# Performance work log

Hardware: AMD Instinct MI355X
Metric: run time of the kernel (lower is better)

The kernel has to match this reference:

```python
import jax, jax.numpy as jnp
import numpy as np

# LLRDenoiser config (init_kwargs): ndim=2, patch W=8, stride S=4, ths=0.1, rand_shift=False
P = 8      # patch size (isotropic)
STRIDE = 4 # patch stride
THS = 0.1  # soft-threshold on singular values
B, C, H, W = 2, 16, 512, 512  # batch, coefficient axis, spatial dims


def setup_inputs() -> dict:
    key = jax.random.key(0)
    x = jax.random.normal(key, (B, C, H, W), dtype=jnp.float32)
    return {"x": x}


def _patch_idx(n, p, s):
    # start indices for sliding windows, inclusive of last full window
    starts = jnp.arange(0, n - p + 1, s)
    return starts[:, None] + jnp.arange(p)[None, :]  # (n_patches, p)


def _llr_denoise(x):
    idx_h = _patch_idx(H, P, STRIDE)  # (nH, P)
    idx_w = _patch_idx(W, P, STRIDE)  # (nW, P)
    nH, nW = idx_h.shape[0], idx_w.shape[0]
    hi = idx_h[:, None, :, None]  # (nH, 1, P, 1)
    wi = idx_w[None, :, None, :]  # (1, nW, 1, P)

    # extract overlapping patches -> (B, C, nH, nW, P, P)
    patches = x[:, :, hi, wi]
    # Casorati matrices per patch: (B, nH*nW, C, P*P)
    mats = patches.transpose(0, 2, 3, 1, 4, 5).reshape(B, nH * nW, C, P * P)

    # batched thin SVD + soft-threshold of singular values
    u, s, vh = jnp.linalg.svd(mats, full_matrices=False)
    s_st = jnp.sign(s) * jnp.maximum(jnp.abs(s) - THS, 0.0)
    mats = (u * s_st[..., None, :]) @ vh

    # back to patch layout (B, C, nH, nW, P, P)
    patches = mats.reshape(B, nH, nW, C, P, P).transpose(0, 3, 1, 2, 4, 5)

    # overlap-add reconstruction, averaged by patch coverage count
    out = jnp.zeros_like(x).at[:, :, hi, wi].add(patches)
    cnt = jnp.zeros((H, W), x.dtype).at[hi[..., 0, :, :] if False else idx_h[:, None, :, None], idx_w[None, :, None, :]].add(1.0)
    return out / cnt


def reference(x):
    return _llr_denoise(x)
```

## Files before the change

kernel.cpp:

```cpp
#include <hip/hip_runtime.h>


#define NBATCH  2
#define NCH     16
#define HDIM    512
#define WDIM    512
#define NPH     127
#define NPW     127
#define NPATCH  (NBATCH * NPH * NPW)
#define NCELL   128
#define THS     0.1f
#define NSIT    8

typedef short bf16x8 __attribute__((ext_vector_type(8)));
typedef float f32x4  __attribute__((ext_vector_type(4)));

#define MFMA(a,b,c) __builtin_amdgcn_mfma_f32_16x16x32_bf16((a),(b),(c),0,0,0)

static __device__ inline short f2bf(float x) {
  return __builtin_bit_cast(short, (__bf16)x);
}
static __device__ inline float blo2f(unsigned int v) {
  return __builtin_bit_cast(float, v << 16);
}
static __device__ inline float bhi2f(unsigned int v) {
  return __builtin_bit_cast(float, v & 0xffff0000u);
}
static __device__ inline unsigned int pack2bf(float lo, float hi) {
  unsigned int a = (unsigned short)f2bf(lo);
  unsigned int b = (unsigned short)f2bf(hi);
  return (b << 16) | a;
}

static __device__ inline int xcd_swz(int b, int nwg) {
  const int q = nwg >> 3, r = nwg & 7;
  const int x = b & 7, lo = b >> 3;
  return (x < r ? x * (q + 1) : r * (q + 1) + (x - r) * q) + lo;
}

static __device__ inline bf16x8 fragc(f32x4 v) {
  bf16x8 r;
  r[0] = f2bf(v[0]); r[1] = f2bf(v[1]); r[2] = f2bf(v[2]); r[3] = f2bf(v[3]);
  r[4] = 0; r[5] = 0; r[6] = 0; r[7] = 0;
  return r;
}

#define ZS_NBLK ((NPATCH + 3) / 4)
__global__ __launch_bounds__(256) void llr_zs(const float* __restrict__ x,
                                              uint2* __restrict__ zs) {
  const int blk = xcd_swz(blockIdx.x, ZS_NBLK);
  const int pid = blk * 4 + (threadIdx.x >> 6);
  if (pid >= NPATCH) return;
  const int bi  = pid / (NPH * NPW);
  const int pr  = pid % (NPH * NPW);
  const int ph  = pr / NPW, pw = pr % NPW;
  const int h0  = ph * 4, w0 = pw * 4;
  const int l   = threadIdx.x & 63;
  const int j   = l & 15;
  const int u   = l >> 4;

  const size_t HW = (size_t)HDIM * WDIM;
  const float* xb = x + (size_t)bi * NCH * HW;

  const float* pb = xb + (size_t)j * HW + (size_t)h0 * WDIM + w0;
  const int dh0 = (u >> 1), dw0 = 4 * (u & 1);
  float4 q0 = *(const float4*)(pb + (size_t)(dh0 + 0) * WDIM + dw0);
  float4 q1 = *(const float4*)(pb + (size_t)(dh0 + 2) * WDIM + dw0);
  float4 q2 = *(const float4*)(pb + (size_t)(dh0 + 4) * WDIM + dw0);
  float4 q3 = *(const float4*)(pb + (size_t)(dh0 + 6) * WDIM + dw0);

  bf16x8 m0, m1;
  m0[0]=f2bf(q0.x); m0[1]=f2bf(q0.y); m0[2]=f2bf(q0.z); m0[3]=f2bf(q0.w);
  m0[4]=f2bf(q1.x); m0[5]=f2bf(q1.y); m0[6]=f2bf(q1.z); m0[7]=f2bf(q1.w);
  m1[0]=f2bf(q2.x); m1[1]=f2bf(q2.y); m1[2]=f2bf(q2.z); m1[3]=f2bf(q2.w);
  m1[4]=f2bf(q3.x); m1[5]=f2bf(q3.y); m1[6]=f2bf(q3.z); m1[7]=f2bf(q3.w);

  f32x4 g = {0.f, 0.f, 0.f, 0.f};
  g = MFMA(m0, m0, g);
  g = MFMA(m1, m1, g);

  float s2 = g[0]*g[0] + g[1]*g[1] + g[2]*g[2] + g[3]*g[3];
  #pragma unroll
  for (int m = 32; m >= 1; m >>= 1) s2 += __shfl_xor(s2, m, 64);

  uint2 wv = {0u, 0u};
  if (s2 > 1e-20f) {
    const float invf  = rsqrtf(s2);
    const float gsc   = 2.0f * invf;
    const float alpha = THS * sqrtf(gsc);

    f32x4 Yc, Zc;
    #pragma unroll
    for (int r = 0; r < 4; ++r) {
      Yc[r] = g[r] * gsc;
      Zc[r] = (4 * u + r == j) ? 1.0f : 0.0f;
    }

    const f32x4 zero = {0.f, 0.f, 0.f, 0.f};
    for (int it = 0; it < NSIT - 1; ++it) {
      bf16x8 yF = fragc(Yc), zF = fragc(Zc);
      f32x4 t  = MFMA(zF, yF, zero);
      bf16x8 tF = fragc(t);
      f32x4 py = MFMA(yF, tF, zero);
      f32x4 pz = MFMA(tF, zF, zero);
      #pragma unroll
      for (int r = 0; r < 4; ++r) {
        Yc[r] = 1.5f * Yc[r] - 0.5f * py[r];
        Zc[r] = 1.5f * Zc[r] - 0.5f * pz[r];
      }
    }
    {
      bf16x8 yF = fragc(Yc), zF = fragc(Zc);
      f32x4 t  = MFMA(zF, yF, zero);
      bf16x8 tF = fragc(t);
      f32x4 pz = MFMA(tF, zF, zero);
      #pragma unroll
      for (int r = 0; r < 4; ++r) Zc[r] = 1.5f * Zc[r] - 0.5f * pz[r];
    }

    wv.x = pack2bf(alpha * Zc[0], alpha * Zc[1]);
    wv.y = pack2bf(alpha * Zc[2], alpha * Zc[3]);
  }
  zs[(size_t)pid * 64 + l] = wv;
}

#define ST_SEG  4
#define ST_NBLK (NBATCH * NCELL * ST_SEG)
__global__ __launch_bounds__(256, 4) void llr_strip(const float* __restrict__ x,
                                                    const uint2* __restrict__ zs,
                                                    float* __restrict__ out) {
  __shared__ unsigned int Wl[32 * 128];

  const int bid = xcd_swz(blockIdx.x, ST_NBLK);
  const int seg = bid & 3;
  const int ci  = (bid >> 2) & 127;
  const int bi  = bid >> 9;
  const int t   = threadIdx.x;
  const int r   = t >> 6;
  const int q2  = t & 63;

  const size_t HW = (size_t)HDIM * WDIM;
  const float* xb = x + (size_t)bi * NCH * HW;
  float* ob = out + (size_t)bi * NCH * HW;

  const int h   = 4 * ci + r;
  const int wpx = seg * 128 + 2 * q2;
  const float* px = xb + (size_t)h * WDIM + wpx;
  float2 xv[16];
  #pragma unroll
  for (int e = 0; e < 16; ++e) xv[e] = *(const float2*)(px + e * HW);

  {
    const int l = t & 63;
    const int u = l >> 4, j = l & 15;
    const float cnth = 2.0f - (ci == 0) - (ci == NCELL - 1);
    const uint2* zb = zs + (size_t)bi * NPH * NPW * 64;
    #pragma unroll
    for (int rho = 0; rho < 8; ++rho) {
      const int c  = rho * 4 + r;
      const int cj = seg * 32 + c;
      float a0 = 0.f, a1 = 0.f, a2 = 0.f, a3 = 0.f;
      #pragma unroll
      for (int dh = 0; dh < 2; ++dh) {
        const int ph = ci - 1 + dh;
        if ((unsigned)ph > (unsigned)(NPH - 1)) continue;
        #pragma unroll
        for (int dw = 0; dw < 2; ++dw) {
          const int pw = cj - 1 + dw;
          if ((unsigned)pw > (unsigned)(NPW - 1)) continue;
          uint2 z = zb[((size_t)ph * NPW + pw) * 64 + l];
          a0 += blo2f(z.x); a1 += bhi2f(z.x);
          a2 += blo2f(z.y); a3 += bhi2f(z.y);
        }
      }
      const float cntw = 2.0f - (cj == 0) - (cj == NCELL - 1);
      const float s = 1.0f / (cnth * cntw);
      const int base = c * 128;
      const int u0 = 8 * u + (j >> 2);
      const int u1 = u0 + 4;
      Wl[base + (((u0 + c) & 31) << 2) + (j & 3)] = pack2bf(s * a0, s * a1);
      Wl[base + (((u1 + c) & 31) << 2) + (j & 3)] = pack2bf(s * a2, s * a3);
    }
  }
  __syncthreads();

  const int cl = q2 >> 1;
  float* po = ob + (size_t)h * WDIM + wpx;
  #pragma unroll
  for (int cp = 0; cp < 8; ++cp) {
    float2 d0 = {0.f, 0.f};
    float2 d1 = {0.f, 0.f};
    #pragma unroll
    for (int k = 0; k < 4; ++k) {
      const uint4 V = *(const uint4*)&Wl[cl * 128 + (((4 * cp + k + cl) & 31) << 2)];
      const unsigned int va[4] = {V.x, V.y, V.z, V.w};
      #pragma unroll
      for (int c = 0; c < 4; ++c) {
        const int e = 4 * k + c;
        const float wlo = blo2f(va[c]);
        const float whi = bhi2f(va[c]);
        d0.x += wlo * xv[e].x; d0.y += wlo * xv[e].y;
        d1.x += whi * xv[e].x; d1.y += whi * xv[e].y;
      }
    }
    const int c0 = 2 * cp, c1 = 2 * cp + 1;
    float2 o0, o1;
    o0.x = xv[c0].x - d0.x; o0.y = xv[c0].y - d0.y;
    o1.x = xv[c1].x - d1.x; o1.y = xv[c1].y - d1.y;
    *(float2*)(po + (size_t)c0 * HW) = o0;
    *(float2*)(po + (size_t)c1 * HW) = o1;
  }
}

extern "C" void kernel_launch(void* const* d_in, const int* in_sizes, int n_in,
                              void* d_out, int out_size, void* d_ws, size_t ws_size,
                              hipStream_t stream) {
  const float* x = (const float*)d_in[0];
  float* out = (float*)d_out;
  uint2* zs = (uint2*)d_ws;

  llr_zs<<<dim3(ZS_NBLK), dim3(256), 0, stream>>>(x, zs);
  llr_strip<<<dim3(ST_NBLK), dim3(256), 0, stream>>>(x, zs, out);
}
```

Before: 48.80 us.

## Share vertical patch-pair sums across neighboring cells in strip kernel

The strip kernel now sums the two vertically adjacent patch matrices once per patch column into a padded shared buffer of 17 columns. Each cell then adds its two horizontal neighbours on the fly, where before every cell gathered four patches separately. This cuts the global loads of the patch matrices from four per cell to about two. Blocks become narrower (8 segments of 64 pixels, one float per thread, 8 blocks per CU in the launch bounds), the XCD swizzle is dropped, and normalisation moves to the output stage. The trade-offs are extra LDS reads and adds in the inner loop, and scalar instead of float2 global accesses.

Result: slower. 49.99 us (+2.4%).

```diff
diff --git a/kernel.cpp b/kernel.cpp
--- a/kernel.cpp
+++ b/kernel.cpp
@@ -124,91 +124,83 @@
   zs[(size_t)pid * 64 + l] = wv;
 }
 
-#define ST_SEG  4
+#define ST_SEG  8
 #define ST_NBLK (NBATCH * NCELL * ST_SEG)
-__global__ __launch_bounds__(256, 4) void llr_strip(const float* __restrict__ x,
+__global__ __launch_bounds__(256, 8) void llr_strip(const float* __restrict__ x,
                                                     const uint2* __restrict__ zs,
                                                     float* __restrict__ out) {
-  __shared__ unsigned int Wl[32 * 128];
-
-  const int bid = xcd_swz(blockIdx.x, ST_NBLK);
-  const int seg = bid & 3;
-  const int ci  = (bid >> 2) & 127;
-  const int bi  = bid >> 9;
+  __shared__ unsigned int RS[17 * 132];
+
+  const int bid = blockIdx.x;
+  const int seg = bid & 7;
+  const int ci  = (bid >> 3) & 127;
+  const int bi  = bid >> 10;
   const int t   = threadIdx.x;
   const int r   = t >> 6;
-  const int q2  = t & 63;
+  const int l   = t & 63;
 
   const size_t HW = (size_t)HDIM * WDIM;
   const float* xb = x + (size_t)bi * NCH * HW;
   float* ob = out + (size_t)bi * NCH * HW;
 
   const int h   = 4 * ci + r;
-  const int wpx = seg * 128 + 2 * q2;
+  const int wpx = seg * 64 + l;
   const float* px = xb + (size_t)h * WDIM + wpx;
-  float2 xv[16];
+  float xv[16];
   #pragma unroll
-  for (int e = 0; e < 16; ++e) xv[e] = *(const float2*)(px + e * HW);
+  for (int e = 0; e < 16; ++e) xv[e] = px[(size_t)e * HW];
 
   {
-    const int l = t & 63;
     const int u = l >> 4, j = l & 15;
-    const float cnth = 2.0f - (ci == 0) - (ci == NCELL - 1);
     const uint2* zb = zs + (size_t)bi * NPH * NPW * 64;
-    #pragma unroll
-    for (int rho = 0; rho < 8; ++rho) {
-      const int c  = rho * 4 + r;
-      const int cj = seg * 32 + c;
-      float a0 = 0.f, a1 = 0.f, a2 = 0.f, a3 = 0.f;
-      #pragma unroll
-      for (int dh = 0; dh < 2; ++dh) {
-        const int ph = ci - 1 + dh;
-        if ((unsigned)ph > (unsigned)(NPH - 1)) continue;
-        #pragma unroll
-        for (int dw = 0; dw < 2; ++dw) {
-          const int pw = cj - 1 + dw;
-          if ((unsigned)pw > (unsigned)(NPW - 1)) continue;
-          uint2 z = zb[((size_t)ph * NPW + pw) * 64 + l];
-          a0 += blo2f(z.x); a1 += bhi2f(z.x);
-          a2 += blo2f(z.y); a3 += bhi2f(z.y);
-        }
-      }
-      const float cntw = 2.0f - (cj == 0) - (cj == NCELL - 1);
-      const float s = 1.0f / (cnth * cntw);
-      const int base = c * 128;
-      const int u0 = 8 * u + (j >> 2);
-      const int u1 = u0 + 4;
-      Wl[base + (((u0 + c) & 31) << 2) + (j & 3)] = pack2bf(s * a0, s * a1);
-      Wl[base + (((u1 + c) & 31) << 2) + (j & 3)] = pack2bf(s * a2, s * a3);
+    const bool vh0 = (ci > 0), vh1 = (ci < NPH);
+    const int ph0c = vh0 ? ci - 1 : 0;
+    const int ph1c = vh1 ? ci : NPH - 1;
+    for (int s = r; s < 17; s += 4) {
+      const int pw = seg * 16 - 1 + s;
+      const bool vw = ((unsigned)pw <= (unsigned)(NPW - 1));
+      const int pwc = vw ? pw : 0;
+      uint2 z0 = zb[((size_t)ph0c * NPW + pwc) * 64 + l];
+      uint2 z1 = zb[((size_t)ph1c * NPW + pwc) * 64 + l];
+      if (!(vw && vh0)) { z0.x = 0u; z0.y = 0u; }
+      if (!(vw && vh1)) { z1.x = 0u; z1.y = 0u; }
+      const float a0 = blo2f(z0.x) + blo2f(z1.x);
+      const float a1 = bhi2f(z0.x) + bhi2f(z1.x);
+      const float a2 = blo2f(z0.y) + blo2f(z1.y);
+      const float a3 = bhi2f(z0.y) + bhi2f(z1.y);
+      RS[s * 132 + 32 * u + j]      = pack2bf(a0, a1);
+      RS[s * 132 + 32 * u + 16 + j] = pack2bf(a2, a3);
     }
   }
   __syncthreads();
 
-  const int cl = q2 >> 1;
+  const int cl = l >> 2;
+  const int cj = seg * 16 + cl;
+  const float cnth = 2.0f - (ci == 0) - (ci == NCELL - 1);
+  const float cntw = 2.0f - (cj == 0) - (cj == NCELL - 1);
+  const float sc = 1.0f / (cnth * cntw);
+
   float* po = ob + (size_t)h * WDIM + wpx;
   #pragma unroll
-  for (int cp = 0; cp < 8; ++cp) {
-    float2 d0 = {0.f, 0.f};
-    float2 d1 = {0.f, 0.f};
+  for (int p = 0; p < 8; ++p) {
+    float d0 = 0.f, d1 = 0.f;
     #pragma unroll
     for (int k = 0; k < 4; ++k) {
-      const uint4 V = *(const uint4*)&Wl[cl * 128 + (((4 * cp + k + cl) & 31) << 2)];
-      const unsigned int va[4] = {V.x, V.y, V.z, V.w};
+      const uint4 A = *(const uint4*)&RS[cl * 132 + 16 * p + 4 * k];
+      const uint4 B = *(const uint4*)&RS[(cl + 1) * 132 + 16 * p + 4 * k];
+      const unsigned int aa[4] = {A.x, A.y, A.z, A.w};
+      const unsigned int bb[4] = {B.x, B.y, B.z, B.w};
       #pragma unroll
       for (int c = 0; c < 4; ++c) {
         const int e = 4 * k + c;
-        const float wlo = blo2f(va[c]);
-        const float whi = bhi2f(va[c]);
-        d0.x += wlo * xv[e].x; d0.y += wlo * xv[e].y;
-        d1.x += whi * xv[e].x; d1.y += whi * xv[e].y;
+        const float wlo = blo2f(aa[c]) + blo2f(bb[c]);
+        const float whi = bhi2f(aa[c]) + bhi2f(bb[c]);
+        d0 += wlo * xv[e];
+        d1 += whi * xv[e];
       }
     }
-    const int c0 = 2 * cp, c1 = 2 * cp + 1;
-    float2 o0, o1;
-    o0.x = xv[c0].x - d0.x; o0.y = xv[c0].y - d0.y;
-    o1.x = xv[c1].x - d1.x; o1.y = xv[c1].y - d1.y;
-    *(float2*)(po + (size_t)c0 * HW) = o0;
-    *(float2*)(po + (size_t)c1 * HW) = o1;
+    po[(size_t)(2 * p) * HW]     = xv[2 * p]     - sc * d0;
+    po[(size_t)(2 * p + 1) * HW] = xv[2 * p + 1] - sc * d1;
   }
 }
 
```
